# Kernel optimization log

Measured on AMD Instinct MI355X. Metric: run time of the kernel, lower is better.

## Reference

```python
import jax, jax.numpy as jnp
import numpy as np

INPUT_DIM = 512
HIDDEN_DIM = 512
B, N = 8, 2048


def setup_inputs() -> dict:
    key = jax.random.key(0)
    ks = jax.random.split(key, 9)
    s_in = 1.0 / np.sqrt(INPUT_DIM)
    s_h = 1.0 / np.sqrt(HIDDEN_DIM)
    return {
        "X": jax.random.normal(ks[0], (B, N, INPUT_DIM), dtype=jnp.float32),
        "Wq": jax.random.uniform(ks[1], (INPUT_DIM, HIDDEN_DIM), minval=-s_in, maxval=s_in),
        "bq": jnp.zeros((HIDDEN_DIM,), jnp.float32),
        "Wk": jax.random.uniform(ks[2], (INPUT_DIM, HIDDEN_DIM), minval=-s_in, maxval=s_in),
        "bk": jnp.zeros((HIDDEN_DIM,), jnp.float32),
        "Wv": jax.random.uniform(ks[3], (INPUT_DIM, HIDDEN_DIM), minval=-s_in, maxval=s_in),
        "bv": jnp.zeros((HIDDEN_DIM,), jnp.float32),
        "Wo": jax.random.uniform(ks[4], (HIDDEN_DIM, INPUT_DIM), minval=-s_h, maxval=s_h),
        "bo": jnp.zeros((INPUT_DIM,), jnp.float32),
        "ln_gamma": jnp.ones((INPUT_DIM,), jnp.float32),
        "ln_beta": jnp.zeros((INPUT_DIM,), jnp.float32),
    }


def reference(X, Wq, bq, Wk, bk, Wv, bv, Wo, bo, ln_gamma, ln_beta):
    q = X @ Wq + bq                      # [B,N,H]
    k = X @ Wk + bk
    v = X @ Wv + bv
    scores = jnp.einsum('bnh,bmh->bnm', q, k) / jnp.sqrt(jnp.float32(HIDDEN_DIM))
    attn = jax.nn.softmax(scores, axis=-1)      # [B,N,N]
    ctx = jnp.einsum('bnm,bmh->bnh', attn, v)   # [B,N,H]
    out = ctx @ Wo + bo + X                      # residual
    mu = jnp.mean(out, axis=-1, keepdims=True)
    var = jnp.var(out, axis=-1, keepdims=True)
    normed = (out - mu) / jnp.sqrt(var + 1e-5)
    return normed * ln_gamma + ln_beta
```

## Files before the change

kernel.cpp:

```cpp
#include <hip/hip_runtime.h>
#include <cstdint>
#include <cstddef>


typedef __bf16 bf16x8 __attribute__((ext_vector_type(8)));
typedef float  f32x4  __attribute__((ext_vector_type(4)));

__device__ __forceinline__ uint16_t f2bf(float f) {
  union { float f; uint32_t u; } v; v.f = f;
  uint32_t r = v.u + 0x7FFFu + ((v.u >> 16) & 1u);
  return (uint16_t)(r >> 16);
}

__device__ __forceinline__ void gld16(const uint16_t* g, uint16_t* l) {
  __builtin_amdgcn_global_load_lds(
      (__attribute__((address_space(1))) void*)(g),
      (__attribute__((address_space(3))) void*)(l), 16, 0, 0);
}

template <int MODE, int BM, int BN>
__global__ __launch_bounds__(256, 2) void gemm_k(
    const uint16_t* __restrict__ A, const uint16_t* __restrict__ Bt,
    void* __restrict__ OutA, uint16_t* __restrict__ OutK,
    uint16_t* __restrict__ OutVT, float* __restrict__ rsum, int K, int lda,
    int ldb, const float* __restrict__ b0, const float* __restrict__ b1,
    const float* __restrict__ b2, float scale) {
  constexpr int MT = BM / 32;
  constexpr int NT = BN / 32;
  constexpr int AI = BM / 64;
  constexpr int BI = BN / 64;
  constexpr int PW = AI + BI;
  __shared__ alignas(16) uint16_t As[3][BM * 32];
  __shared__ alignas(16) uint16_t Bs[3][BN * 32];

  const int tid = threadIdx.x;
  const int w = tid >> 6, lane = tid & 63;
  const int wm = w >> 1, wn = w & 1;

  const int gx = gridDim.x, gy = gridDim.y;
  const int nwg = gx * gy * gridDim.z;
  const int hw = blockIdx.x + gx * (blockIdx.y + gy * blockIdx.z);
  const int lg = (hw & 7) * (nwg >> 3) + (hw >> 3);
  const int bx = lg % gx, byz = lg / gx;
  const int by = byz % gy, z = byz / gy;

  const int m0 = by * BM, n0 = bx * BN;

  const uint16_t* Ab = A;
  const uint16_t* Bb = Bt;
  if (MODE == 1) { Ab += (size_t)z * 2048 * 512;  Bb += (size_t)z * 2048 * 512; }
  if (MODE == 2) { Ab += (size_t)z * 2048 * 2048; Bb += (size_t)z * 512 * 2048; }

  const int kc = (((lane & 3) ^ ((lane >> 2) & 3) ^ (lane >> 4)) * 8);
  const int rbA = w * (BM / 4);
  const int rbB = w * (BN / 4);
  const uint16_t* gA = Ab + (size_t)(m0 + rbA + (lane >> 2)) * lda + kc;
  const uint16_t* gB = Bb + (size_t)(n0 + rbB + (lane >> 2)) * ldb + kc;

  f32x4 acc[MT][NT];
#pragma unroll
  for (int i = 0; i < MT; i++)
#pragma unroll
    for (int j = 0; j < NT; j++) acc[i][j] = (f32x4){0.f, 0.f, 0.f, 0.f};

  const int lr = lane & 15, q4 = lane >> 4;
  const int swz = (((lane >> 4) ^ (lr & 3) ^ (lr >> 2)) * 8);
  const int iters = K >> 5;

  auto stage = [&](int t, int buf) {
    const int k0 = t * 32;
#pragma unroll
    for (int j = 0; j < AI; j++)
      gld16(gA + k0 + (size_t)(j * 16) * lda, &As[buf][(rbA + j * 16) * 32]);
#pragma unroll
    for (int j = 0; j < BI; j++)
      gld16(gB + k0 + (size_t)(j * 16) * ldb, &Bs[buf][(rbB + j * 16) * 32]);
  };

  auto compute = [&](int buf) {
    bf16x8 af[MT], bfr[NT];
#pragma unroll
    for (int t = 0; t < MT; t++)
      af[t] = *(const bf16x8*)&As[buf][(wm * (BM / 2) + t * 16 + lr) * 32 + swz];
#pragma unroll
    for (int t = 0; t < NT; t++)
      bfr[t] = *(const bf16x8*)&Bs[buf][(wn * (BN / 2) + t * 16 + lr) * 32 + swz];
#pragma unroll
    for (int nt = 0; nt < NT; nt++)
#pragma unroll
      for (int mt = 0; mt < MT; mt++)
        acc[mt][nt] = __builtin_amdgcn_mfma_f32_16x16x32_bf16(
            af[mt], bfr[nt], acc[mt][nt], 0, 0, 0);
  };

  stage(0, 0);
  stage(1, 1);
  int buf = 0;
  for (int i = 0; i < iters - 1; ++i) {
    asm volatile("s_waitcnt vmcnt(%0)" ::"i"(PW) : "memory");
    __builtin_amdgcn_s_barrier();
    if (i + 2 < iters) stage(i + 2, (buf + 2 >= 3) ? buf - 1 : buf + 2);
    compute(buf);
    buf = (buf == 2) ? 0 : buf + 1;
  }
  asm volatile("s_waitcnt vmcnt(0)" ::: "memory");
  __builtin_amdgcn_s_barrier();
  compute(buf);

  if (MODE == 1) {
    uint16_t* Sp = (uint16_t*)OutA + (size_t)z * 2048 * 2048;
#pragma unroll
    for (int mt = 0; mt < MT; mt++) {
      float rp[4] = {0.f, 0.f, 0.f, 0.f};
#pragma unroll
      for (int nt = 0; nt < NT; nt++) {
#pragma unroll
        for (int i = 0; i < 4; i++) {
          const int row = m0 + wm * (BM / 2) + mt * 16 + q4 * 4 + i;
          const int col = n0 + wn * (BN / 2) + nt * 16 + lr;
          const float e = __expf(acc[mt][nt][i] * scale);
          Sp[(size_t)row * 2048 + col] = f2bf(e);
          rp[i] += e;
        }
      }
#pragma unroll
      for (int i = 0; i < 4; i++) {
        float p = rp[i];
        p += __shfl_xor(p, 1); p += __shfl_xor(p, 2);
        p += __shfl_xor(p, 4); p += __shfl_xor(p, 8);
        if (lr == 0) {
          const int row = m0 + wm * (BM / 2) + mt * 16 + q4 * 4 + i;
          atomicAdd(&rsum[z * 2048 + row], p);
        }
      }
    }
  } else if (MODE == 2) {
#pragma unroll
    for (int mt = 0; mt < MT; mt++) {
#pragma unroll
      for (int i = 0; i < 4; i++) {
        const int row = m0 + wm * (BM / 2) + mt * 16 + q4 * 4 + i;
        const float sc = 1.0f / rsum[z * 2048 + row];
#pragma unroll
        for (int nt = 0; nt < NT; nt++) {
          const int col = n0 + wn * (BN / 2) + nt * 16 + lr;
          ((uint16_t*)OutA)[((size_t)z * 2048 + row) * 512 + col] =
              f2bf(acc[mt][nt][i] * sc);
        }
      }
    }
  } else {
#pragma unroll
    for (int mt = 0; mt < MT; mt++) {
#pragma unroll
      for (int nt = 0; nt < NT; nt++) {
#pragma unroll
        for (int i = 0; i < 4; i++) {
          const int row = m0 + wm * (BM / 2) + mt * 16 + q4 * 4 + i;
          const int col = n0 + wn * (BN / 2) + nt * 16 + lr;
          const float v = acc[mt][nt][i];
          const int which = col >> 9, c = col & 511;
          if (which == 0) {
            ((uint16_t*)OutA)[(size_t)row * 512 + c] = f2bf(v + b0[c]);
          } else if (which == 1) {
            OutK[(size_t)row * 512 + c] = f2bf(v + b1[c]);
          } else {
            OutVT[(size_t)(row >> 11) * (512 * 2048) + (size_t)c * 2048 +
                  (row & 2047)] = f2bf(v + b2[c]);
          }
        }
      }
    }
  }
}

template <int BM, int BN, int WM, int WN>
__global__ __launch_bounds__(512, 4) void gemmf_k(
    const uint16_t* __restrict__ A, const uint16_t* __restrict__ Bt,
    void* __restrict__ OutA, int K, int lda, int ldb,
    const float* __restrict__ b0, const float* __restrict__ b1,
    const float* __restrict__ b2, const float* __restrict__ Xres) {
  constexpr int MT = (BM / WM) / 16;
  constexpr int NT = (BN / WN) / 16;
  static_assert(MT == 4 && NT == 4, "wave tile must be 64x64");
  constexpr int AI = (BM >= 128) ? BM / 128 : 1;
  constexpr int BI = BN / 128;
  constexpr int PW = AI + BI;
  __shared__ alignas(16) uint16_t As[3][BM * 32];
  __shared__ alignas(16) uint16_t Bs[3][BN * 32];

  const int tid = threadIdx.x;
  const int w = tid >> 6, lane = tid & 63;
  const int wm = w / WN, wn = w % WN;

  const int gx = gridDim.x, gy = gridDim.y;
  const int nwg = gx * gy * gridDim.z;
  const int hw = blockIdx.x + gx * (blockIdx.y + gy * blockIdx.z);
  const int lg = (hw & 7) * (nwg >> 3) + (hw >> 3);
  const int bx = lg % gx, byz = lg / gx;
  const int by = byz % gy;

  const int m0 = by * BM, n0 = bx * BN;

  const uint16_t* Ab = A;
  const uint16_t* Bb = Bt;

  const int kc = (((lane & 3) ^ ((lane >> 2) & 3) ^ (lane >> 4)) * 8);
  const int rbA = (BM >= 128) ? w * (BM / 8) : (w & 3) * 16;
  const int rbB = w * (BN / 8);
  const uint16_t* gA = Ab + (size_t)(m0 + rbA + (lane >> 2)) * lda + kc;
  const uint16_t* gB = Bb + (size_t)(n0 + rbB + (lane >> 2)) * ldb + kc;

  f32x4 acc[MT][NT];
#pragma unroll
  for (int i = 0; i < MT; i++)
#pragma unroll
    for (int j = 0; j < NT; j++) acc[i][j] = (f32x4){0.f, 0.f, 0.f, 0.f};

  const int lr = lane & 15, q4 = lane >> 4;
  const int swz = (((lane >> 4) ^ (lr & 3) ^ (lr >> 2)) * 8);
  const int iters = K >> 5;

  auto stage = [&](int t, int buf) {
    const int k0 = t * 32;
#pragma unroll
    for (int j = 0; j < AI; j++)
      gld16(gA + k0 + (size_t)(j * 16) * lda, &As[buf][(rbA + j * 16) * 32]);
#pragma unroll
    for (int j = 0; j < BI; j++)
      gld16(gB + k0 + (size_t)(j * 16) * ldb, &Bs[buf][(rbB + j * 16) * 32]);
  };

  auto compute = [&](int buf) {
    bf16x8 af[MT], bfr[NT];
#pragma unroll
    for (int t = 0; t < MT; t++)
      af[t] = *(const bf16x8*)&As[buf][(wm * (BM / WM) + t * 16 + lr) * 32 + swz];
#pragma unroll
    for (int t = 0; t < NT; t++)
      bfr[t] = *(const bf16x8*)&Bs[buf][(wn * (BN / WN) + t * 16 + lr) * 32 + swz];
#pragma unroll
    for (int nt = 0; nt < NT; nt++)
#pragma unroll
      for (int mt = 0; mt < MT; mt++)
        acc[mt][nt] = __builtin_amdgcn_mfma_f32_16x16x32_bf16(
            af[mt], bfr[nt], acc[mt][nt], 0, 0, 0);
  };

  stage(0, 0);
  stage(1, 1);
  int buf = 0;
  for (int i = 0; i < iters - 1; ++i) {
    asm volatile("s_waitcnt vmcnt(%0)" ::"i"(PW) : "memory");
    __builtin_amdgcn_s_barrier();
    if (i + 2 < iters) stage(i + 2, (buf + 2 >= 3) ? buf - 1 : buf + 2);
    compute(buf);
    buf = (buf == 2) ? 0 : buf + 1;
  }
  asm volatile("s_waitcnt vmcnt(0)" ::: "memory");
  __builtin_amdgcn_s_barrier();
  compute(buf);

  __shared__ float redS[8][64];
  __shared__ float redQ[8][64];
  float* Op = (float*)OutA;
  __syncthreads();
#pragma unroll
  for (int mt = 0; mt < MT; mt++) {
#pragma unroll
    for (int i = 0; i < 4; i++) {
      const int rl = mt * 16 + q4 * 4 + i;
      const int row = m0 + rl;
      float ps = 0.f, pq = 0.f;
#pragma unroll
      for (int nt = 0; nt < NT; nt++) {
        const int col = wn * 64 + nt * 16 + lr;
        float v = acc[mt][nt][i] + b0[col] + Xres[(size_t)row * 512 + col];
        acc[mt][nt][i] = v;
        ps += v; pq += v * v;
      }
      ps += __shfl_xor(ps, 1); pq += __shfl_xor(pq, 1);
      ps += __shfl_xor(ps, 2); pq += __shfl_xor(pq, 2);
      ps += __shfl_xor(ps, 4); pq += __shfl_xor(pq, 4);
      ps += __shfl_xor(ps, 8); pq += __shfl_xor(pq, 8);
      if (lr == 0) { redS[w][rl] = ps; redQ[w][rl] = pq; }
    }
  }
  __syncthreads();
#pragma unroll
  for (int mt = 0; mt < MT; mt++) {
#pragma unroll
    for (int i = 0; i < 4; i++) {
      const int rl = mt * 16 + q4 * 4 + i;
      const int row = m0 + rl;
      float s8 = 0.f, q8 = 0.f;
#pragma unroll
      for (int ww = 0; ww < 8; ww++) { s8 += redS[ww][rl]; q8 += redQ[ww][rl]; }
      const float mean = s8 * (1.f / 512.f);
      const float var = q8 * (1.f / 512.f) - mean * mean;
      const float rstd = rsqrtf(var + 1e-5f);
#pragma unroll
      for (int nt = 0; nt < NT; nt++) {
        const int col = wn * 64 + nt * 16 + lr;
        Op[(size_t)row * 512 + col] =
            (acc[mt][nt][i] - mean) * rstd * b1[col] + b2[col];
      }
    }
  }
}

__global__ __launch_bounds__(256) void cvt_all_k(
    const float* __restrict__ X, uint16_t* __restrict__ Xb,
    const float* __restrict__ Wq, const float* __restrict__ Wk,
    const float* __restrict__ Wv, const float* __restrict__ Wo,
    uint16_t* __restrict__ Wt, float* __restrict__ rsum) {
  const int i = blockIdx.x * 256 + threadIdx.x;
  const float4 f = ((const float4*)X)[i];
  uint32_t lo = (uint32_t)f2bf(f.x) | ((uint32_t)f2bf(f.y) << 16);
  uint32_t hi = (uint32_t)f2bf(f.z) | ((uint32_t)f2bf(f.w) << 16);
  ((uint2*)Xb)[i] = make_uint2(lo, hi);
  if (i < 16384) rsum[i] = 0.f;
  if (i < 2048 * 512) {
    const int n = i >> 9, kk = i & 511;
    const int which = n >> 9, c = n & 511;
    const float* W =
        (which == 0) ? Wq : (which == 1) ? Wk : (which == 2) ? Wv : Wo;
    Wt[i] = f2bf(W[kk * 512 + c]);
  }
}

extern "C" void kernel_launch(void* const* d_in, const int* in_sizes, int n_in,
                              void* d_out, int out_size, void* d_ws,
                              size_t ws_size, hipStream_t stream) {
  const float* X     = (const float*)d_in[0];
  const float* Wq    = (const float*)d_in[1];
  const float* bq    = (const float*)d_in[2];
  const float* Wk    = (const float*)d_in[3];
  const float* bk    = (const float*)d_in[4];
  const float* Wv    = (const float*)d_in[5];
  const float* bv    = (const float*)d_in[6];
  const float* Wo    = (const float*)d_in[7];
  const float* bo    = (const float*)d_in[8];
  const float* gamma = (const float*)d_in[9];
  const float* beta  = (const float*)d_in[10];
  float* out = (float*)d_out;

  char* ws = (char*)d_ws;
  uint16_t* S    = (uint16_t*)(ws);
  uint16_t* Xb   = (uint16_t*)(ws);
  uint16_t* Wt   = (uint16_t*)(ws + 67108864);
  uint16_t* q    = (uint16_t*)(ws + 69206016);
  uint16_t* kb   = (uint16_t*)(ws + 85983232);
  uint16_t* vT   = (uint16_t*)(ws + 102760448);
  float*    rsum = (float*)(ws + 119537664);
  uint16_t* ctx  = q;

  cvt_all_k<<<dim3(8192), dim3(256), 0, stream>>>(X, Xb, Wq, Wk, Wv, Wo, Wt,
                                                  rsum);
  gemm_k<0, 128, 128><<<dim3(12, 128, 1), dim3(256), 0, stream>>>(
      Xb, Wt, (void*)q, kb, vT, nullptr, 512, 512, 512, bq, bk, bv, 1.f);
  gemm_k<1, 128, 128><<<dim3(16, 16, 8), dim3(256), 0, stream>>>(
      q, kb, (void*)S, nullptr, nullptr, rsum, 512, 512, 512, nullptr, nullptr,
      nullptr, 0.044194173824159216f);
  gemm_k<2, 64, 128><<<dim3(4, 32, 8), dim3(256), 0, stream>>>(
      S, vT, (void*)ctx, nullptr, nullptr, rsum, 2048, 2048, 2048, nullptr,
      nullptr, nullptr, 1.f);
  gemmf_k<64, 512, 1, 8><<<dim3(1, 256, 1), dim3(512), 0, stream>>>(
      ctx, Wt + 1536 * 512, (void*)out, 512, 512, 512, bo, gamma, beta, X);
}
```

Baseline: 320.1 us.

## Fuse QK^T, exp and PV into a single flash-style attention kernel

Replaces the separate score GEMM (which wrote a bf16 B×N×N matrix of exponentials plus atomic row sums) and the PV GEMM with one attention kernel. Each block keeps Q in registers, streams 64-key K/V tiles through LDS, computes exp scores into a small LDS tile and accumulates PV directly, then normalises by row sums at the end. This removes the large score-matrix round trip through HBM and the atomics. In exchange it uses no running max (it relies on bounded scores, as the old code did), launches only 256 blocks with heavy LDS and register use at occupancy 1, and has limited overlap between loads and compute.

```diff
diff --git a/kernel.cpp b/kernel.cpp
--- a/kernel.cpp
+++ b/kernel.cpp
@@ -18,13 +18,153 @@
       (__attribute__((address_space(3))) void*)(l), 16, 0, 0);
 }
 
-template <int MODE, int BM, int BN>
+__global__ __launch_bounds__(256, 1) void attn_k(
+    const uint16_t* __restrict__ qg, const uint16_t* __restrict__ kg,
+    const uint16_t* __restrict__ vTg, uint16_t* __restrict__ ctx,
+    float scale) {
+  __shared__ alignas(16) uint16_t Ks[64 * 512];
+  __shared__ alignas(16) uint16_t Vs[512 * 64];
+  __shared__ alignas(16) uint16_t Es[64 * 64];
+  __shared__ float rs[64][2];
+
+  const int tid = threadIdx.x;
+  const int w = tid >> 6, lane = tid & 63;
+  const int wm = w >> 1, wn = w & 1;
+  const int lr = lane & 15, q4 = lane >> 4;
+  const int lr7 = lr & 7;
+  const int l3 = lane >> 3, l7 = lane & 7;
+
+  const int hw = blockIdx.x + 32 * blockIdx.y;
+  const int lg = (hw & 7) * 32 + (hw >> 3);
+  const int bx = lg & 31, z = lg >> 5;
+  const int q0 = bx * 64;
+
+  const uint16_t* qb = qg + ((size_t)z * 2048 + q0) * 512;
+  const uint16_t* kb = kg + (size_t)z * 2048 * 512;
+  const uint16_t* vb = vTg + (size_t)z * 512 * 2048;
+
+  bf16x8 qf[2][16];
+#pragma unroll
+  for (int mt = 0; mt < 2; mt++)
+#pragma unroll
+    for (int ks = 0; ks < 16; ks++)
+      qf[mt][ks] = *(const bf16x8*)&qb[(size_t)(wm * 32 + mt * 16 + lr) * 512 +
+                                       ks * 32 + q4 * 8];
+  asm volatile("s_waitcnt vmcnt(0)" ::: "memory");
+
+  f32x4 acc[4][8];
+#pragma unroll
+  for (int mt = 0; mt < 4; mt++)
+#pragma unroll
+    for (int ht = 0; ht < 8; ht++) acc[mt][ht] = (f32x4){0.f, 0.f, 0.f, 0.f};
+  float psum[2][4] = {{0.f, 0.f, 0.f, 0.f}, {0.f, 0.f, 0.f, 0.f}};
+
+  for (int kt = 0; kt < 32; ++kt) {
+    const int kv0 = kt * 64;
+#pragma unroll
+    for (int j = 0; j < 16; j++) {
+      const int r = w * 16 + j;
+      gld16(kb + (size_t)(kv0 + r) * 512 + (lane ^ (r & 7)) * 8, &Ks[r * 512]);
+    }
+#pragma unroll
+    for (int j = 0; j < 16; j++) {
+      const int g = w * 16 + j;
+      gld16(vb + (size_t)(g * 8 + l3) * 2048 + kv0 + (l7 ^ l3) * 8,
+            &Vs[g * 512]);
+    }
+    asm volatile("s_waitcnt vmcnt(16)" ::: "memory");
+    __builtin_amdgcn_s_barrier();
+
+    f32x4 sacc[2][2];
+#pragma unroll
+    for (int mt = 0; mt < 2; mt++)
+#pragma unroll
+      for (int nt = 0; nt < 2; nt++) sacc[mt][nt] = (f32x4){0.f, 0.f, 0.f, 0.f};
+#pragma unroll
+    for (int ks = 0; ks < 16; ks++) {
+      bf16x8 kf[2];
+#pragma unroll
+      for (int nt = 0; nt < 2; nt++) {
+        const int r = wn * 32 + nt * 16 + lr;
+        kf[nt] = *(const bf16x8*)&Ks[r * 512 + ((ks * 4 + q4) ^ lr7) * 8];
+      }
+#pragma unroll
+      for (int nt = 0; nt < 2; nt++)
+#pragma unroll
+        for (int mt = 0; mt < 2; mt++)
+          sacc[mt][nt] = __builtin_amdgcn_mfma_f32_16x16x32_bf16(
+              qf[mt][ks], kf[nt], sacc[mt][nt], 0, 0, 0);
+    }
+#pragma unroll
+    for (int mt = 0; mt < 2; mt++)
+#pragma unroll
+      for (int nt = 0; nt < 2; nt++)
+#pragma unroll
+        for (int i = 0; i < 4; i++) {
+          const float e = __expf(sacc[mt][nt][i] * scale);
+          const int r = wm * 32 + mt * 16 + q4 * 4 + i;
+          const int c = wn * 32 + nt * 16 + lr;
+          Es[r * 64 + (((c >> 3) ^ (r & 7)) * 8) + lr7] = f2bf(e);
+          psum[mt][i] += e;
+        }
+    asm volatile("s_waitcnt lgkmcnt(0)" ::: "memory");
+    asm volatile("s_waitcnt vmcnt(0)" ::: "memory");
+    __builtin_amdgcn_s_barrier();
+
+#pragma unroll
+    for (int ks = 0; ks < 2; ks++) {
+      bf16x8 ef[4];
+#pragma unroll
+      for (int mt = 0; mt < 4; mt++)
+        ef[mt] = *(const bf16x8*)&Es[(mt * 16 + lr) * 64 +
+                                     ((ks * 4 + q4) ^ lr7) * 8];
+#pragma unroll
+      for (int ht = 0; ht < 8; ht++) {
+        const int h = w * 128 + ht * 16 + lr;
+        const bf16x8 vf =
+            *(const bf16x8*)&Vs[h * 64 + ((ks * 4 + q4) ^ lr7) * 8];
+#pragma unroll
+        for (int mt = 0; mt < 4; mt++)
+          acc[mt][ht] = __builtin_amdgcn_mfma_f32_16x16x32_bf16(
+              ef[mt], vf, acc[mt][ht], 0, 0, 0);
+      }
+    }
+    __builtin_amdgcn_s_barrier();
+  }
+
+#pragma unroll
+  for (int mt = 0; mt < 2; mt++)
+#pragma unroll
+    for (int i = 0; i < 4; i++) {
+      float p = psum[mt][i];
+      p += __shfl_xor(p, 1); p += __shfl_xor(p, 2);
+      p += __shfl_xor(p, 4); p += __shfl_xor(p, 8);
+      if (lr == 0) rs[wm * 32 + mt * 16 + q4 * 4 + i][wn] = p;
+    }
+  __syncthreads();
+
+#pragma unroll
+  for (int mt = 0; mt < 4; mt++)
+#pragma unroll
+    for (int i = 0; i < 4; i++) {
+      const int r = mt * 16 + q4 * 4 + i;
+      const float inv = 1.0f / (rs[r][0] + rs[r][1]);
+#pragma unroll
+      for (int ht = 0; ht < 8; ht++) {
+        const int col = w * 128 + ht * 16 + lr;
+        ctx[((size_t)z * 2048 + q0 + r) * 512 + col] =
+            f2bf(acc[mt][ht][i] * inv);
+      }
+    }
+}
+
+template <int BM, int BN>
 __global__ __launch_bounds__(256, 2) void gemm_k(
     const uint16_t* __restrict__ A, const uint16_t* __restrict__ Bt,
-    void* __restrict__ OutA, uint16_t* __restrict__ OutK,
-    uint16_t* __restrict__ OutVT, float* __restrict__ rsum, int K, int lda,
-    int ldb, const float* __restrict__ b0, const float* __restrict__ b1,
-    const float* __restrict__ b2, float scale) {
+    uint16_t* __restrict__ OutQ, uint16_t* __restrict__ OutK,
+    uint16_t* __restrict__ OutVT, int K, int lda, int ldb,
+    const float* __restrict__ b0, const float* __restrict__ b1,
+    const float* __restrict__ b2) {
   constexpr int MT = BM / 32;
   constexpr int NT = BN / 32;
   constexpr int AI = BM / 64;
@@ -38,24 +178,18 @@
   const int wm = w >> 1, wn = w & 1;
 
   const int gx = gridDim.x, gy = gridDim.y;
-  const int nwg = gx * gy * gridDim.z;
-  const int hw = blockIdx.x + gx * (blockIdx.y + gy * blockIdx.z);
+  const int nwg = gx * gy;
+  const int hw = blockIdx.x + gx * blockIdx.y;
   const int lg = (hw & 7) * (nwg >> 3) + (hw >> 3);
-  const int bx = lg % gx, byz = lg / gx;
-  const int by = byz % gy, z = byz / gy;
+  const int bx = lg % gx, by = lg / gx;
 
   const int m0 = by * BM, n0 = bx * BN;
-
-  const uint16_t* Ab = A;
-  const uint16_t* Bb = Bt;
-  if (MODE == 1) { Ab += (size_t)z * 2048 * 512;  Bb += (size_t)z * 2048 * 512; }
-  if (MODE == 2) { Ab += (size_t)z * 2048 * 2048; Bb += (size_t)z * 512 * 2048; }
 
   const int kc = (((lane & 3) ^ ((lane >> 2) & 3) ^ (lane >> 4)) * 8);
   const int rbA = w * (BM / 4);
   const int rbB = w * (BN / 4);
-  const uint16_t* gA = Ab + (size_t)(m0 + rbA + (lane >> 2)) * lda + kc;
-  const uint16_t* gB = Bb + (size_t)(n0 + rbB + (lane >> 2)) * ldb + kc;
+  const uint16_t* gA = A + (size_t)(m0 + rbA + (lane >> 2)) * lda + kc;
+  const uint16_t* gB = Bt + (size_t)(n0 + rbB + (lane >> 2)) * ldb + kc;
 
   f32x4 acc[MT][NT];
 #pragma unroll
@@ -107,67 +241,23 @@
   __builtin_amdgcn_s_barrier();
   compute(buf);
 
-  if (MODE == 1) {
-    uint16_t* Sp = (uint16_t*)OutA + (size_t)z * 2048 * 2048;
-#pragma unroll
-    for (int mt = 0; mt < MT; mt++) {
-      float rp[4] = {0.f, 0.f, 0.f, 0.f};
-#pragma unroll
-      for (int nt = 0; nt < NT; nt++) {
-#pragma unroll
-        for (int i = 0; i < 4; i++) {
-          const int row = m0 + wm * (BM / 2) + mt * 16 + q4 * 4 + i;
-          const int col = n0 + wn * (BN / 2) + nt * 16 + lr;
-          const float e = __expf(acc[mt][nt][i] * scale);
-          Sp[(size_t)row * 2048 + col] = f2bf(e);
-          rp[i] += e;
-        }
-      }
-#pragma unroll
-      for (int i = 0; i < 4; i++) {
-        float p = rp[i];
-        p += __shfl_xor(p, 1); p += __shfl_xor(p, 2);
-        p += __shfl_xor(p, 4); p += __shfl_xor(p, 8);
-        if (lr == 0) {
-          const int row = m0 + wm * (BM / 2) + mt * 16 + q4 * 4 + i;
-          atomicAdd(&rsum[z * 2048 + row], p);
-        }
-      }
-    }
-  } else if (MODE == 2) {
-#pragma unroll
-    for (int mt = 0; mt < MT; mt++) {
+#pragma unroll
+  for (int mt = 0; mt < MT; mt++) {
+#pragma unroll
+    for (int nt = 0; nt < NT; nt++) {
 #pragma unroll
       for (int i = 0; i < 4; i++) {
         const int row = m0 + wm * (BM / 2) + mt * 16 + q4 * 4 + i;
-        const float sc = 1.0f / rsum[z * 2048 + row];
-#pragma unroll
-        for (int nt = 0; nt < NT; nt++) {
-          const int col = n0 + wn * (BN / 2) + nt * 16 + lr;
-          ((uint16_t*)OutA)[((size_t)z * 2048 + row) * 512 + col] =
-              f2bf(acc[mt][nt][i] * sc);
-        }
-      }
-    }
-  } else {
-#pragma unroll
-    for (int mt = 0; mt < MT; mt++) {
-#pragma unroll
-      for (int nt = 0; nt < NT; nt++) {
-#pragma unroll
-        for (int i = 0; i < 4; i++) {
-          const int row = m0 + wm * (BM / 2) + mt * 16 + q4 * 4 + i;
-          const int col = n0 + wn * (BN / 2) + nt * 16 + lr;
-          const float v = acc[mt][nt][i];
-          const int which = col >> 9, c = col & 511;
-          if (which == 0) {
-            ((uint16_t*)OutA)[(size_t)row * 512 + c] = f2bf(v + b0[c]);
-          } else if (which == 1) {
-            OutK[(size_t)row * 512 + c] = f2bf(v + b1[c]);
-          } else {
-            OutVT[(size_t)(row >> 11) * (512 * 2048) + (size_t)c * 2048 +
-                  (row & 2047)] = f2bf(v + b2[c]);
-          }
+        const int col = n0 + wn * (BN / 2) + nt * 16 + lr;
+        const float v = acc[mt][nt][i];
+        const int which = col >> 9, c = col & 511;
+        if (which == 0) {
+          OutQ[(size_t)row * 512 + c] = f2bf(v + b0[c]);
+        } else if (which == 1) {
+          OutK[(size_t)row * 512 + c] = f2bf(v + b1[c]);
+        } else {
+          OutVT[(size_t)(row >> 11) * (512 * 2048) + (size_t)c * 2048 +
+                (row & 2047)] = f2bf(v + b2[c]);
         }
       }
     }
@@ -194,22 +284,18 @@
   const int wm = w / WN, wn = w % WN;
 
   const int gx = gridDim.x, gy = gridDim.y;
-  const int nwg = gx * gy * gridDim.z;
-  const int hw = blockIdx.x + gx * (blockIdx.y + gy * blockIdx.z);
+  const int nwg = gx * gy;
+  const int hw = blockIdx.x + gx * blockIdx.y;
   const int lg = (hw & 7) * (nwg >> 3) + (hw >> 3);
-  const int bx = lg % gx, byz = lg / gx;
-  const int by = byz % gy;
+  const int bx = lg % gx, by = lg / gx;
 
   const int m0 = by * BM, n0 = bx * BN;
-
-  const uint16_t* Ab = A;
-  const uint16_t* Bb = Bt;
 
   const int kc = (((lane & 3) ^ ((lane >> 2) & 3) ^ (lane >> 4)) * 8);
   const int rbA = (BM >= 128) ? w * (BM / 8) : (w & 3) * 16;
   const int rbB = w * (BN / 8);
-  const uint16_t* gA = Ab + (size_t)(m0 + rbA + (lane >> 2)) * lda + kc;
-  const uint16_t* gB = Bb + (size_t)(n0 + rbB + (lane >> 2)) * ldb + kc;
+  const uint16_t* gA = A + (size_t)(m0 + rbA + (lane >> 2)) * lda + kc;
+  const uint16_t* gB = Bt + (size_t)(n0 + rbB + (lane >> 2)) * ldb + kc;
 
   f32x4 acc[MT][NT];
 #pragma unroll
@@ -313,13 +399,12 @@
     const float* __restrict__ X, uint16_t* __restrict__ Xb,
     const float* __restrict__ Wq, const float* __restrict__ Wk,
     const float* __restrict__ Wv, const float* __restrict__ Wo,
-    uint16_t* __restrict__ Wt, float* __restrict__ rsum) {
+    uint16_t* __restrict__ Wt) {
   const int i = blockIdx.x * 256 + threadIdx.x;
   const float4 f = ((const float4*)X)[i];
   uint32_t lo = (uint32_t)f2bf(f.x) | ((uint32_t)f2bf(f.y) << 16);
   uint32_t hi = (uint32_t)f2bf(f.z) | ((uint32_t)f2bf(f.w) << 16);
   ((uint2*)Xb)[i] = make_uint2(lo, hi);
-  if (i < 16384) rsum[i] = 0.f;
   if (i < 2048 * 512) {
     const int n = i >> 9, kk = i & 511;
     const int which = n >> 9, c = n & 511;
@@ -346,25 +431,20 @@
   float* out = (float*)d_out;
 
   char* ws = (char*)d_ws;
-  uint16_t* S    = (uint16_t*)(ws);
   uint16_t* Xb   = (uint16_t*)(ws);
   uint16_t* Wt   = (uint16_t*)(ws + 67108864);
   uint16_t* q    = (uint16_t*)(ws + 69206016);
   uint16_t* kb   = (uint16_t*)(ws + 85983232);
   uint16_t* vT   = (uint16_t*)(ws + 102760448);
-  float*    rsum = (float*)(ws + 119537664);
   uint16_t* ctx  = q;
 
-  cvt_all_k<<<dim3(8192), dim3(256), 0, stream>>>(X, Xb, Wq, Wk, Wv, Wo, Wt,
-                                                  rsum);
-  gemm_k<0, 128, 128><<<dim3(12, 128, 1), dim3(256), 0, stream>>>(
-      Xb, Wt, (void*)q, kb, vT, nullptr, 512, 512, 512, bq, bk, bv, 1.f);
-  gemm_k<1, 128, 128><<<dim3(16, 16, 8), dim3(256), 0, stream>>>(
-      q, kb, (void*)S, nullptr, nullptr, rsum, 512, 512, 512, nullptr, nullptr,
-      nullptr, 0.044194173824159216f);
-  gemm_k<2, 64, 128><<<dim3(4, 32, 8), dim3(256), 0, stream>>>(
-      S, vT, (void*)ctx, nullptr, nullptr, rsum, 2048, 2048, 2048, nullptr,
-      nullptr, nullptr, 1.f);
-  gemmf_k<64, 512, 1, 8><<<dim3(1, 256, 1), dim3(512), 0, stream>>>(
+  ctx = Xb;
+
+  cvt_all_k<<<dim3(8192), dim3(256), 0, stream>>>(X, Xb, Wq, Wk, Wv, Wo, Wt);
+  gemm_k<128, 128><<<dim3(12, 128), dim3(256), 0, stream>>>(
+      Xb, Wt, q, kb, vT, 512, 512, 512, bq, bk, bv);
+  attn_k<<<dim3(32, 8), dim3(256), 0, stream>>>(
+      q, kb, vT, ctx, 0.044194173824159216f);
+  gemmf_k<64, 512, 1, 8><<<dim3(1, 256), dim3(512), 0, stream>>>(
       ctx, Wt + 1536 * 512, (void*)out, 512, 512, 512, bo, gamma, beta, X);
 }
```

Result: no change. 325.9 us (+1.8%).
